# Kernel tuning notes

Hardware: AMD Instinct MI355X
Metric: run time of the kernel (lower is better)

Reference implementation:

```python
import jax, jax.numpy as jnp
import numpy as np

DT = 0.001
TAU_INV = 1.0 / 0.006   # tau_mem_inv == tau_syn_inv for both cells
V_TH = 1.0              # norse defaults: v_leak=0, v_reset=0


def heaviside(x):
    return (x > 0).astype(x.dtype)


def setup_inputs() -> dict:
    key = jax.random.key(0)
    k1, k2, k3 = jax.random.split(key, 3)
    T, B, I, H, O = 128, 2048, 64, 256, 16
    inp = jax.random.normal(k1, (T, B, I), dtype=jnp.float32)
    # torch.nn.Linear default init ~ U(-1/sqrt(fan_in), 1/sqrt(fan_in))
    w1 = jax.random.uniform(k2, (H, I), jnp.float32, -1.0, 1.0) / np.sqrt(I)
    w2 = jax.random.uniform(k3, (O, H), jnp.float32, -1.0, 1.0) / np.sqrt(H)
    return {"input": inp, "w1": w1, "w2": w2}


def _snn_forward(inp, w1, w2):
    B = inp.shape[1]
    H, O = w1.shape[0], w2.shape[0]
    decay = 1.0 - DT * TAU_INV

    def step(carry, x_t):
        v1, i1, v2, i2 = carry
        # LIF cell (hidden layer)
        g1 = x_t @ w1.T                              # [B, H]
        v_dec = v1 + DT * TAU_INV * (i1 - v1)        # Euler membrane update
        i_dec = i1 * decay                           # synaptic decay
        z = heaviside(v_dec - V_TH)                  # spikes
        v1n = (1.0 - z) * v_dec                      # reset to 0 where spiked
        i1n = i_dec + g1
        # LI cell (readout)
        g2 = z @ w2.T                                # [B, O]
        v2n = v2 + DT * TAU_INV * (i2 - v2)
        i2n = i2 * decay + g2
        return (v1n, i1n, v2n, i2n), (z, v2n)

    init = (jnp.zeros((B, H), inp.dtype), jnp.zeros((B, H), inp.dtype),
            jnp.zeros((B, O), inp.dtype), jnp.zeros((B, O), inp.dtype))
    _, (zs, ys) = jax.lax.scan(step, init, inp)
    score = jnp.max(ys, axis=0)                      # amax over time -> [B, O]
    spikes_mean = jnp.mean(jnp.sum(zs, axis=(0, 2)))
    return score, spikes_mean


def reference(input, w1, w2):
    return _snn_forward(input, w1, w2)
```

## Files before the change

kernel.cpp:

```cpp
#include <hip/hip_runtime.h>
#include <hip/hip_bf16.h>

#define T_STEPS 128
#define BATCH   2048
#define IN_F    64
#define HID     256
#define OUT_F   16
#define CH      8
#define NCH     (T_STEPS / CH)
#define SLAB    (BATCH * OUT_F)
#define SPART_OFS (32u * 1024u * 1024u)

typedef __attribute__((ext_vector_type(8))) short bf16x8;
typedef __attribute__((ext_vector_type(4))) float f32x4;
typedef unsigned short u16;
typedef unsigned int   u32;

__device__ __forceinline__ u16 f2bf(float f) {
    union { __hip_bfloat16 h; u16 u; } cv;
    cv.h = __float2bfloat16(f);
    return cv.u;
}
__device__ __forceinline__ float bf2f(u16 h) {
    return __uint_as_float(((u32)h) << 16);
}
__device__ __forceinline__ bf16x8 pack8(float4 a, float4 b) {
    bf16x8 r;
    r[0] = (short)f2bf(a.x); r[1] = (short)f2bf(a.y);
    r[2] = (short)f2bf(a.z); r[3] = (short)f2bf(a.w);
    r[4] = (short)f2bf(b.x); r[5] = (short)f2bf(b.y);
    r[6] = (short)f2bf(b.z); r[7] = (short)f2bf(b.w);
    return r;
}

__device__ __forceinline__ void lds_barrier() {
    __builtin_amdgcn_sched_barrier(0);
    asm volatile("s_waitcnt lgkmcnt(0)" ::: "memory");
    __builtin_amdgcn_sched_barrier(0);
    __builtin_amdgcn_s_barrier();
    __builtin_amdgcn_sched_barrier(0);
}

__global__ void __launch_bounds__(512, 2)
snn_l1_kernel(const float* __restrict__ x, const float* __restrict__ w1,
              const float* __restrict__ w2, u16* __restrict__ g2p,
              u32* __restrict__ spart)
{
    const int tid  = threadIdx.x;
    const int lane = tid & 63;
    const int wv   = tid >> 6;
    const int hi   = lane >> 4;
    const int l15  = lane & 15;
    const int tile = blockIdx.x & 127;
    const int half = blockIdx.x >> 7;
    const int row0 = tile * 16;
    const int hbase = half * 128 + wv * 16;

    __shared__ __attribute__((aligned(16))) u16 xl[2][CH * 2 * 512];
    __shared__ __attribute__((aligned(16))) u16 zb[2][CH * 4 * 512];

    const f32x4 zf = {0.f, 0.f, 0.f, 0.f};
    const float dt_tau = (float)(0.001 * (1.0 / 0.006));
    const float decay  = (float)(1.0 - 0.001 * (1.0 / 0.006));

    bf16x8 w1f[2];
#pragma unroll
    for (int kh = 0; kh < 2; ++kh) {
        const float* src = &w1[(hbase + l15) * IN_F + kh * 32 + hi * 8];
        w1f[kh] = pack8(*(const float4*)src, *(const float4*)(src + 4));
    }
    bf16x8 w2f[4];
#pragma unroll
    for (int kt = 0; kt < 4; ++kt) {
        const int k0 = half * 128 + kt * 32 + hi * 8;
        w2f[kt] = pack8(*(const float4*)&w2[l15 * HID + k0],
                        *(const float4*)&w2[l15 * HID + k0 + 4]);
    }

    const size_t cstride = (size_t)CH * BATCH * IN_F;
    const float* gp[2];
    int wofs[2];
#pragma unroll
    for (int j = 0; j < 2; ++j) {
        const int u  = tid + 512 * j;
        const int s  = u >> 7, r7 = u & 127;
        const int f  = r7 >> 6, chi = (r7 >> 4) & 3, cl = r7 & 15;
        wofs[j] = (s * 2 + f) * 512 + (chi * 16 + cl) * 8;
        gp[j]   = x + ((size_t)s * BATCH + row0 + cl) * IN_F + f * 32 + chi * 8;
    }
    float4 ra[2], rb[2];
#pragma unroll
    for (int j = 0; j < 2; ++j) {
        ra[j] = *(const float4*)gp[j];
        rb[j] = *(const float4*)(gp[j] + 4);
        *(bf16x8*)&xl[0][wofs[j]] = pack8(ra[j], rb[j]);
    }
#pragma unroll
    for (int j = 0; j < 2; ++j) {
        ra[j] = *(const float4*)(gp[j] + cstride);
        rb[j] = *(const float4*)(gp[j] + cstride + 4);
        gp[j] += 2 * cstride;
    }

    const int zwkey = ((l15 >> 3) << 5) | (((hi >> 1) & 1) << 4);
    const int zwofs = (wv >> 1) * 512
                    + (((((wv & 1) * 2 + (hi >> 1)) * 16 + l15) * 8 + (hi & 1) * 4)
                       ^ zwkey);
    const int zrkey = ((l15 >> 3) << 5) | ((hi & 1) << 4);
    const int zrofs = ((hi * 16 + l15) * 8) ^ zrkey;

    f32x4 v1 = zf, i1 = zf;
    int wcnt = 0;

    auto phaseA = [&](int k) {
        const int kb = k & 1;
        const u16* xb = &xl[kb][0];
        u16* zw = &zb[kb][0];
        if (k + 1 < NCH) {
#pragma unroll
            for (int j = 0; j < 2; ++j)
                *(bf16x8*)&xl[kb ^ 1][wofs[j]] = pack8(ra[j], rb[j]);
        }
        if (k + 2 < NCH) {
#pragma unroll
            for (int j = 0; j < 2; ++j) {
                ra[j] = *(const float4*)gp[j];
                rb[j] = *(const float4*)(gp[j] + 4);
                gp[j] += cstride;
            }
        }
        bf16x8 xfa[CH], xfb[CH];
#pragma unroll
        for (int s = 0; s < 3; ++s) {
            xfa[s] = *(const bf16x8*)&xb[(s * 2 + 0) * 512 + lane * 8];
            xfb[s] = *(const bf16x8*)&xb[(s * 2 + 1) * 512 + lane * 8];
        }
        uint2 zi[CH];
#pragma unroll
        for (int s = 0; s < CH; ++s) {
            if (s + 3 < CH) {
                xfa[s + 3] = *(const bf16x8*)&xb[((s + 3) * 2 + 0) * 512 + lane * 8];
                xfb[s + 3] = *(const bf16x8*)&xb[((s + 3) * 2 + 1) * 512 + lane * 8];
            }
            f32x4 g1 = __builtin_amdgcn_mfma_f32_16x16x32_bf16(w1f[0], xfa[s], zf, 0, 0, 0);
            g1 = __builtin_amdgcn_mfma_f32_16x16x32_bf16(w1f[1], xfb[s], g1, 0, 0, 0);

            const f32x4 vd = v1 + dt_tau * (i1 - v1);
            bool sp[4];
#pragma unroll
            for (int r = 0; r < 4; ++r) {
                sp[r] = vd[r] > 1.0f;
                v1[r] = sp[r] ? 0.f : vd[r];
                wcnt += __popcll(__ballot(sp[r]));
            }
            i1 = i1 * decay + g1;
            zi[s].x = (sp[0] ? 0x3F80u : 0u) | (sp[1] ? 0x3F800000u : 0u);
            zi[s].y = (sp[2] ? 0x3F80u : 0u) | (sp[3] ? 0x3F800000u : 0u);
        }
#pragma unroll
        for (int s = 0; s < CH; ++s)
            *(uint2*)&zw[s * 2048 + zwofs] = zi[s];
    };

    auto phaseC = [&](int c) {
        const int cb = c & 1;
        const u16* zr = &zb[cb][wv * 2048];
        const bf16x8 z0 = *(const bf16x8*)&zr[0 * 512 + zrofs];
        const bf16x8 z1 = *(const bf16x8*)&zr[1 * 512 + zrofs];
        const bf16x8 z2 = *(const bf16x8*)&zr[2 * 512 + zrofs];
        const bf16x8 z3 = *(const bf16x8*)&zr[3 * 512 + zrofs];
        __builtin_amdgcn_s_setprio(1);
        f32x4 ga = __builtin_amdgcn_mfma_f32_16x16x32_bf16(z0, w2f[0], zf, 0, 0, 0);
        f32x4 gb = __builtin_amdgcn_mfma_f32_16x16x32_bf16(z1, w2f[1], zf, 0, 0, 0);
        ga = __builtin_amdgcn_mfma_f32_16x16x32_bf16(z2, w2f[2], ga, 0, 0, 0);
        gb = __builtin_amdgcn_mfma_f32_16x16x32_bf16(z3, w2f[3], gb, 0, 0, 0);
        __builtin_amdgcn_s_setprio(0);
        const f32x4 g2 = ga + gb;
        u16* dst = g2p + (size_t)half * (T_STEPS * SLAB)
                 + (size_t)(c * CH + wv) * SLAB + (row0 + 4 * hi) * OUT_F + l15;
#pragma unroll
        for (int r = 0; r < 4; ++r) dst[r * OUT_F] = f2bf(g2[r]);
    };

    lds_barrier();
    phaseA(0);

    for (int c = 0; c < NCH; ++c) {
        lds_barrier();
        if ((wv & 1) == 0) {
            if (c + 1 < NCH) phaseA(c + 1);
            phaseC(c);
        } else {
            phaseC(c);
            if (c + 1 < NCH) phaseA(c + 1);
        }
    }

    if (lane == 0) spart[blockIdx.x * 8 + wv] = (u32)wcnt;
}

__global__ void __launch_bounds__(256)
snn_li_kernel(const u16* __restrict__ g2p, const u32* __restrict__ spart,
              float* __restrict__ out)
{
    const int gid = blockIdx.x * 256 + threadIdx.x;
    const u16* p0 = g2p + gid;
    const u16* p1 = p0 + (size_t)T_STEPS * SLAB;
    const float dt_tau = (float)(0.001 * (1.0 / 0.006));
    const float decay  = (float)(1.0 - 0.001 * (1.0 / 0.006));
    float v2 = 0.f, i2 = 0.f, ymax = -1e30f;
#pragma unroll 8
    for (int t = 0; t < T_STEPS; ++t) {
        const size_t o = (size_t)t * SLAB;
        const float g = bf2f(p0[o]) + bf2f(p1[o]);
        v2 = fmaf(dt_tau, i2 - v2, v2);
        ymax = fmaxf(ymax, v2);
        i2 = i2 * decay + g;
    }
    out[gid] = ymax;

    if (blockIdx.x == 0) {
        u32 s = 0;
#pragma unroll
        for (int i = 0; i < 8; ++i) s += spart[threadIdx.x * 8 + i];
#pragma unroll
        for (int m = 1; m < 64; m <<= 1) s += __shfl_xor(s, m, 64);
        __shared__ u32 sb[4];
        if ((threadIdx.x & 63) == 0) sb[threadIdx.x >> 6] = s;
        __syncthreads();
        if (threadIdx.x == 0)
            out[BATCH * OUT_F] =
                (float)(sb[0] + sb[1] + sb[2] + sb[3]) * (1.0f / BATCH);
    }
}

extern "C" void kernel_launch(void* const* d_in, const int* in_sizes, int n_in,
                              void* d_out, int out_size, void* d_ws, size_t ws_size,
                              hipStream_t stream) {
    const float* x  = (const float*)d_in[0];
    const float* w1 = (const float*)d_in[1];
    const float* w2 = (const float*)d_in[2];
    float* out = (float*)d_out;
    u16* g2p   = (u16*)d_ws;
    u32* spart = (u32*)((char*)d_ws + SPART_OFS);

    hipLaunchKernelGGL(snn_l1_kernel, dim3(256), dim3(512), 0, stream,
                       x, w1, w2, g2p, spart);
    hipLaunchKernelGGL(snn_li_kernel, dim3(BATCH * OUT_F / 256), dim3(256), 0,
                       stream, g2p, spart, out);
}
```

Measured before the change: 44.55 us.

## Specialize waves into LIF-compute producers and load/readout consumers

Splits the 8 waves of each block into two roles. Four waves each run the hidden-layer recurrence for 32 hidden units, interleaving two independent MFMA/LIF chains. The other four waves stage the input into LDS and run the readout MFMAs and g2 stores one chunk behind. This replaces the symmetric per-wave phase interleaving with producer/consumer warp specialization, so global loads and readout overlap with the serial LIF recurrence. The cost is more registers per LIF wave, an imbalance between the two roles, and one extra barrier iteration per block.

```diff
diff --git a/kernel.cpp b/kernel.cpp
--- a/kernel.cpp
+++ b/kernel.cpp
@@ -54,7 +54,6 @@
     const int tile = blockIdx.x & 127;
     const int half = blockIdx.x >> 7;
     const int row0 = tile * 16;
-    const int hbase = half * 128 + wv * 16;
 
     __shared__ __attribute__((aligned(16))) u16 xl[2][CH * 2 * 512];
     __shared__ __attribute__((aligned(16))) u16 zb[2][CH * 4 * 512];
@@ -62,141 +61,171 @@
     const f32x4 zf = {0.f, 0.f, 0.f, 0.f};
     const float dt_tau = (float)(0.001 * (1.0 / 0.006));
     const float decay  = (float)(1.0 - 0.001 * (1.0 / 0.006));
-
-    bf16x8 w1f[2];
-#pragma unroll
-    for (int kh = 0; kh < 2; ++kh) {
-        const float* src = &w1[(hbase + l15) * IN_F + kh * 32 + hi * 8];
-        w1f[kh] = pack8(*(const float4*)src, *(const float4*)(src + 4));
+    const size_t cstride = (size_t)CH * BATCH * IN_F;
+
+
+    if (wv < 4) {
+        const int p = wv;
+        bf16x8 w1f[2][2];
+#pragma unroll
+        for (int tau = 0; tau < 2; ++tau)
+#pragma unroll
+            for (int kh = 0; kh < 2; ++kh) {
+                const int col = half * 128 + p * 32 + tau * 16 + l15;
+                const float* src = &w1[col * IN_F + kh * 32 + hi * 8];
+                w1f[tau][kh] = pack8(*(const float4*)src, *(const float4*)(src + 4));
+            }
+        const int zwkey = ((l15 >> 3) << 5) | (((hi >> 1) & 1) << 4);
+        int zwofs[2];
+#pragma unroll
+        for (int tau = 0; tau < 2; ++tau) {
+            const int w = 2 * p + tau;
+            zwofs[tau] = (w >> 1) * 512
+                       + (((((w & 1) * 2 + (hi >> 1)) * 16 + l15) * 8 + (hi & 1) * 4)
+                          ^ zwkey);
+        }
+        f32x4 v1a = zf, i1a = zf, v1b = zf, i1b = zf;
+        int wcnt = 0;
+
+        lds_barrier();
+        for (int c = 0; c <= NCH; ++c) {
+            if (c < NCH) {
+                const int kb = c & 1;
+                const u16* xb = &xl[kb][0];
+                u16* zw = &zb[kb][0];
+                bf16x8 xfa[CH], xfb[CH];
+#pragma unroll
+                for (int s = 0; s < 3; ++s) {
+                    xfa[s] = *(const bf16x8*)&xb[(s * 2 + 0) * 512 + lane * 8];
+                    xfb[s] = *(const bf16x8*)&xb[(s * 2 + 1) * 512 + lane * 8];
+                }
+                uint2 zia[CH], zib[CH];
+#pragma unroll
+                for (int s = 0; s < CH; ++s) {
+                    if (s + 3 < CH) {
+                        xfa[s + 3] = *(const bf16x8*)&xb[((s + 3) * 2 + 0) * 512 + lane * 8];
+                        xfb[s + 3] = *(const bf16x8*)&xb[((s + 3) * 2 + 1) * 512 + lane * 8];
+                    }
+                    f32x4 ga = __builtin_amdgcn_mfma_f32_16x16x32_bf16(w1f[0][0], xfa[s], zf, 0, 0, 0);
+                    ga = __builtin_amdgcn_mfma_f32_16x16x32_bf16(w1f[0][1], xfb[s], ga, 0, 0, 0);
+                    f32x4 gb = __builtin_amdgcn_mfma_f32_16x16x32_bf16(w1f[1][0], xfa[s], zf, 0, 0, 0);
+                    gb = __builtin_amdgcn_mfma_f32_16x16x32_bf16(w1f[1][1], xfb[s], gb, 0, 0, 0);
+
+                    {
+                        const f32x4 vd = v1a + dt_tau * (i1a - v1a);
+                        bool sp[4];
+#pragma unroll
+                        for (int r = 0; r < 4; ++r) {
+                            sp[r] = vd[r] > 1.0f;
+                            v1a[r] = sp[r] ? 0.f : vd[r];
+                            wcnt += __popcll(__ballot(sp[r]));
+                        }
+                        i1a = i1a * decay + ga;
+                        zia[s].x = (sp[0] ? 0x3F80u : 0u) | (sp[1] ? 0x3F800000u : 0u);
+                        zia[s].y = (sp[2] ? 0x3F80u : 0u) | (sp[3] ? 0x3F800000u : 0u);
+                    }
+                    {
+                        const f32x4 vd = v1b + dt_tau * (i1b - v1b);
+                        bool sp[4];
+#pragma unroll
+                        for (int r = 0; r < 4; ++r) {
+                            sp[r] = vd[r] > 1.0f;
+                            v1b[r] = sp[r] ? 0.f : vd[r];
+                            wcnt += __popcll(__ballot(sp[r]));
+                        }
+                        i1b = i1b * decay + gb;
+                        zib[s].x = (sp[0] ? 0x3F80u : 0u) | (sp[1] ? 0x3F800000u : 0u);
+                        zib[s].y = (sp[2] ? 0x3F80u : 0u) | (sp[3] ? 0x3F800000u : 0u);
+                    }
+                }
+#pragma unroll
+                for (int s = 0; s < CH; ++s) {
+                    *(uint2*)&zw[s * 2048 + zwofs[0]] = zia[s];
+                    *(uint2*)&zw[s * 2048 + zwofs[1]] = zib[s];
+                }
+            }
+            lds_barrier();
+        }
+        if (lane == 0) spart[blockIdx.x * 4 + p] = (u32)wcnt;
+    } else {
+        const int q = wv - 4;
+        bf16x8 w2f[4];
+#pragma unroll
+        for (int kt = 0; kt < 4; ++kt) {
+            const int k0 = half * 128 + kt * 32 + hi * 8;
+            w2f[kt] = pack8(*(const float4*)&w2[l15 * HID + k0],
+                            *(const float4*)&w2[l15 * HID + k0 + 4]);
+        }
+        const int zrkey = ((l15 >> 3) << 5) | ((hi & 1) << 4);
+        const int zrofs = ((hi * 16 + l15) * 8) ^ zrkey;
+
+        const int ct = tid - 256;
+        const float* gp[4];
+        int wofs[4];
+#pragma unroll
+        for (int j = 0; j < 4; ++j) {
+            const int u  = ct + 256 * j;
+            const int s  = u >> 7, r7 = u & 127;
+            const int f  = r7 >> 6, chi = (r7 >> 4) & 3, cl = r7 & 15;
+            wofs[j] = (s * 2 + f) * 512 + (chi * 16 + cl) * 8;
+            gp[j]   = x + ((size_t)s * BATCH + row0 + cl) * IN_F + f * 32 + chi * 8;
+        }
+        float4 ra[4], rb[4];
+#pragma unroll
+        for (int j = 0; j < 4; ++j) {
+            ra[j] = *(const float4*)gp[j];
+            rb[j] = *(const float4*)(gp[j] + 4);
+            *(bf16x8*)&xl[0][wofs[j]] = pack8(ra[j], rb[j]);
+        }
+#pragma unroll
+        for (int j = 0; j < 4; ++j) {
+            ra[j] = *(const float4*)(gp[j] + cstride);
+            rb[j] = *(const float4*)(gp[j] + cstride + 4);
+            gp[j] += 2 * cstride;
+        }
+
+        lds_barrier();
+        for (int c = 0; c <= NCH; ++c) {
+            if (c + 1 < NCH) {
+#pragma unroll
+                for (int j = 0; j < 4; ++j)
+                    *(bf16x8*)&xl[(c + 1) & 1][wofs[j]] = pack8(ra[j], rb[j]);
+            }
+            if (c + 2 < NCH) {
+#pragma unroll
+                for (int j = 0; j < 4; ++j) {
+                    ra[j] = *(const float4*)gp[j];
+                    rb[j] = *(const float4*)(gp[j] + 4);
+                    gp[j] += cstride;
+                }
+            }
+            if (c >= 1) {
+                const int cb = (c - 1) & 1;
+#pragma unroll
+                for (int e = 0; e < 2; ++e) {
+                    const int s = q * 2 + e;
+                    const u16* zr = &zb[cb][s * 2048];
+                    const bf16x8 z0 = *(const bf16x8*)&zr[0 * 512 + zrofs];
+                    const bf16x8 z1 = *(const bf16x8*)&zr[1 * 512 + zrofs];
+                    const bf16x8 z2 = *(const bf16x8*)&zr[2 * 512 + zrofs];
+                    const bf16x8 z3 = *(const bf16x8*)&zr[3 * 512 + zrofs];
+                    __builtin_amdgcn_s_setprio(1);
+                    f32x4 ga = __builtin_amdgcn_mfma_f32_16x16x32_bf16(z0, w2f[0], zf, 0, 0, 0);
+                    f32x4 gb = __builtin_amdgcn_mfma_f32_16x16x32_bf16(z1, w2f[1], zf, 0, 0, 0);
+                    ga = __builtin_amdgcn_mfma_f32_16x16x32_bf16(z2, w2f[2], ga, 0, 0, 0);
+                    gb = __builtin_amdgcn_mfma_f32_16x16x32_bf16(z3, w2f[3], gb, 0, 0, 0);
+                    __builtin_amdgcn_s_setprio(0);
+                    const f32x4 g2 = ga + gb;
+                    const int t = (c - 1) * CH + s;
+                    u16* dst = g2p + (size_t)half * (T_STEPS * SLAB)
+                             + (size_t)t * SLAB + (row0 + 4 * hi) * OUT_F + l15;
+#pragma unroll
+                    for (int r = 0; r < 4; ++r) dst[r * OUT_F] = f2bf(g2[r]);
+                }
+            }
+            lds_barrier();
+        }
     }
-    bf16x8 w2f[4];
-#pragma unroll
-    for (int kt = 0; kt < 4; ++kt) {
-        const int k0 = half * 128 + kt * 32 + hi * 8;
-        w2f[kt] = pack8(*(const float4*)&w2[l15 * HID + k0],
-                        *(const float4*)&w2[l15 * HID + k0 + 4]);
-    }
-
-    const size_t cstride = (size_t)CH * BATCH * IN_F;
-    const float* gp[2];
-    int wofs[2];
-#pragma unroll
-    for (int j = 0; j < 2; ++j) {
-        const int u  = tid + 512 * j;
-        const int s  = u >> 7, r7 = u & 127;
-        const int f  = r7 >> 6, chi = (r7 >> 4) & 3, cl = r7 & 15;
-        wofs[j] = (s * 2 + f) * 512 + (chi * 16 + cl) * 8;
-        gp[j]   = x + ((size_t)s * BATCH + row0 + cl) * IN_F + f * 32 + chi * 8;
-    }
-    float4 ra[2], rb[2];
-#pragma unroll
-    for (int j = 0; j < 2; ++j) {
-        ra[j] = *(const float4*)gp[j];
-        rb[j] = *(const float4*)(gp[j] + 4);
-        *(bf16x8*)&xl[0][wofs[j]] = pack8(ra[j], rb[j]);
-    }
-#pragma unroll
-    for (int j = 0; j < 2; ++j) {
-        ra[j] = *(const float4*)(gp[j] + cstride);
-        rb[j] = *(const float4*)(gp[j] + cstride + 4);
-        gp[j] += 2 * cstride;
-    }
-
-    const int zwkey = ((l15 >> 3) << 5) | (((hi >> 1) & 1) << 4);
-    const int zwofs = (wv >> 1) * 512
-                    + (((((wv & 1) * 2 + (hi >> 1)) * 16 + l15) * 8 + (hi & 1) * 4)
-                       ^ zwkey);
-    const int zrkey = ((l15 >> 3) << 5) | ((hi & 1) << 4);
-    const int zrofs = ((hi * 16 + l15) * 8) ^ zrkey;
-
-    f32x4 v1 = zf, i1 = zf;
-    int wcnt = 0;
-
-    auto phaseA = [&](int k) {
-        const int kb = k & 1;
-        const u16* xb = &xl[kb][0];
-        u16* zw = &zb[kb][0];
-        if (k + 1 < NCH) {
-#pragma unroll
-            for (int j = 0; j < 2; ++j)
-                *(bf16x8*)&xl[kb ^ 1][wofs[j]] = pack8(ra[j], rb[j]);
-        }
-        if (k + 2 < NCH) {
-#pragma unroll
-            for (int j = 0; j < 2; ++j) {
-                ra[j] = *(const float4*)gp[j];
-                rb[j] = *(const float4*)(gp[j] + 4);
-                gp[j] += cstride;
-            }
-        }
-        bf16x8 xfa[CH], xfb[CH];
-#pragma unroll
-        for (int s = 0; s < 3; ++s) {
-            xfa[s] = *(const bf16x8*)&xb[(s * 2 + 0) * 512 + lane * 8];
-            xfb[s] = *(const bf16x8*)&xb[(s * 2 + 1) * 512 + lane * 8];
-        }
-        uint2 zi[CH];
-#pragma unroll
-        for (int s = 0; s < CH; ++s) {
-            if (s + 3 < CH) {
-                xfa[s + 3] = *(const bf16x8*)&xb[((s + 3) * 2 + 0) * 512 + lane * 8];
-                xfb[s + 3] = *(const bf16x8*)&xb[((s + 3) * 2 + 1) * 512 + lane * 8];
-            }
-            f32x4 g1 = __builtin_amdgcn_mfma_f32_16x16x32_bf16(w1f[0], xfa[s], zf, 0, 0, 0);
-            g1 = __builtin_amdgcn_mfma_f32_16x16x32_bf16(w1f[1], xfb[s], g1, 0, 0, 0);
-
-            const f32x4 vd = v1 + dt_tau * (i1 - v1);
-            bool sp[4];
-#pragma unroll
-            for (int r = 0; r < 4; ++r) {
-                sp[r] = vd[r] > 1.0f;
-                v1[r] = sp[r] ? 0.f : vd[r];
-                wcnt += __popcll(__ballot(sp[r]));
-            }
-            i1 = i1 * decay + g1;
-            zi[s].x = (sp[0] ? 0x3F80u : 0u) | (sp[1] ? 0x3F800000u : 0u);
-            zi[s].y = (sp[2] ? 0x3F80u : 0u) | (sp[3] ? 0x3F800000u : 0u);
-        }
-#pragma unroll
-        for (int s = 0; s < CH; ++s)
-            *(uint2*)&zw[s * 2048 + zwofs] = zi[s];
-    };
-
-    auto phaseC = [&](int c) {
-        const int cb = c & 1;
-        const u16* zr = &zb[cb][wv * 2048];
-        const bf16x8 z0 = *(const bf16x8*)&zr[0 * 512 + zrofs];
-        const bf16x8 z1 = *(const bf16x8*)&zr[1 * 512 + zrofs];
-        const bf16x8 z2 = *(const bf16x8*)&zr[2 * 512 + zrofs];
-        const bf16x8 z3 = *(const bf16x8*)&zr[3 * 512 + zrofs];
-        __builtin_amdgcn_s_setprio(1);
-        f32x4 ga = __builtin_amdgcn_mfma_f32_16x16x32_bf16(z0, w2f[0], zf, 0, 0, 0);
-        f32x4 gb = __builtin_amdgcn_mfma_f32_16x16x32_bf16(z1, w2f[1], zf, 0, 0, 0);
-        ga = __builtin_amdgcn_mfma_f32_16x16x32_bf16(z2, w2f[2], ga, 0, 0, 0);
-        gb = __builtin_amdgcn_mfma_f32_16x16x32_bf16(z3, w2f[3], gb, 0, 0, 0);
-        __builtin_amdgcn_s_setprio(0);
-        const f32x4 g2 = ga + gb;
-        u16* dst = g2p + (size_t)half * (T_STEPS * SLAB)
-                 + (size_t)(c * CH + wv) * SLAB + (row0 + 4 * hi) * OUT_F + l15;
-#pragma unroll
-        for (int r = 0; r < 4; ++r) dst[r * OUT_F] = f2bf(g2[r]);
-    };
-
-    lds_barrier();
-    phaseA(0);
-
-    for (int c = 0; c < NCH; ++c) {
-        lds_barrier();
-        if ((wv & 1) == 0) {
-            if (c + 1 < NCH) phaseA(c + 1);
-            phaseC(c);
-        } else {
-            phaseC(c);
-            if (c + 1 < NCH) phaseA(c + 1);
-        }
-    }
-
-    if (lane == 0) spart[blockIdx.x * 8 + wv] = (u32)wcnt;
 }
 
 __global__ void __launch_bounds__(256)
@@ -222,7 +251,7 @@
     if (blockIdx.x == 0) {
         u32 s = 0;
 #pragma unroll
-        for (int i = 0; i < 8; ++i) s += spart[threadIdx.x * 8 + i];
+        for (int i = 0; i < 4; ++i) s += spart[threadIdx.x * 4 + i];
 #pragma unroll
         for (int m = 1; m < 64; m <<= 1) s += __shfl_xor(s, m, 64);
         __shared__ u32 sb[4];
```

Result: slower. 46.90 us (+5.3%).
